# Kernel tuning notes

Measured on AMD Instinct MI355X. Metric: run time of the kernel, lower is better.

The kernel has to match this reference:

```python
import jax, jax.numpy as jnp
import numpy as np

N, M, D = 4096, 8192, 512

def setup_inputs() -> dict:
    key = jax.random.key(0)
    k1, k2, k3, k4 = jax.random.split(key, 4)
    X = jax.random.normal(k1, (N, D), dtype=jnp.float32)
    SV = jax.random.normal(k2, (M, D), dtype=jnp.float32)
    DC = jax.random.normal(k3, (1, M), dtype=jnp.float32)
    IC = jax.random.normal(k4, (1,), dtype=jnp.float32)
    gamma = jnp.float32(1.0 / D)
    return {"X": X, "SV": SV, "DC": DC, "IC": IC, "gamma": gamma}

def reference(X, SV, DC, IC, gamma):
    # Squared pairwise L2 distances via GEMM expansion (same math as
    # ||SV - x||^2 without materializing the [N, M, D] broadcast tensor):
    # d2[n, m] = ||x_n||^2 + ||sv_m||^2 - 2 * x_n . sv_m
    x2 = jnp.sum(X * X, axis=1)          # [N]
    sv2 = jnp.sum(SV * SV, axis=1)       # [M]
    cross = jnp.einsum("nd,md->nm", X, SV)  # [N, M]
    d2 = jnp.maximum(x2[:, None] + sv2[None, :] - 2.0 * cross, 0.0)
    k = jnp.exp(-gamma * d2)             # RBF kernel values [N, M]
    # Weighted reduction over support vectors + intercept -> decision values [N]
    return jnp.sum(k * DC, axis=1) + IC
```

## Files before the change

kernel.cpp:

```cpp
#include <hip/hip_runtime.h>
#include <stdint.h>

#define NN 4096
#define MM 8192
#define DD 512
#define KT 8

typedef __bf16 bf16x8 __attribute__((ext_vector_type(8)));
typedef __bf16 bf16x4 __attribute__((ext_vector_type(4)));
typedef float f32x4 __attribute__((ext_vector_type(4)));
typedef float f32x16 __attribute__((ext_vector_type(16)));

__device__ __forceinline__ void load_lds16(const void* g, void* l) {
  __builtin_amdgcn_global_load_lds(
      (const __attribute__((address_space(1))) unsigned int*)g,
      (__attribute__((address_space(3))) unsigned int*)l, 16, 0, 0);
}

__global__ __launch_bounds__(256) void convert_norm_kernel(
    const float* __restrict__ X, const float* __restrict__ SV,
    __bf16* __restrict__ Xb, __bf16* __restrict__ SVb,
    float* __restrict__ x2, float* __restrict__ sv2,
    float* __restrict__ out, const float* __restrict__ IC) {
  int wid = blockIdx.x * 4 + (threadIdx.x >> 6);
  int lane = threadIdx.x & 63;
  const float* src;
  __bf16* dst;
  float* nrm;
  if (wid < NN) {
    src = X + (size_t)wid * DD;
    dst = Xb + (size_t)wid * DD;
    nrm = x2 + wid;
    if (lane == 0) out[wid] = IC[0];
  } else {
    int r = wid - NN;
    src = SV + (size_t)r * DD;
    dst = SVb + (size_t)r * DD;
    nrm = sv2 + r;
  }
  const f32x4* s = (const f32x4*)src;
  f32x4 a = s[lane];
  f32x4 b = s[lane + 64];
  float sum = a.x * a.x + a.y * a.y + a.z * a.z + a.w * a.w +
              b.x * b.x + b.y * b.y + b.z * b.z + b.w * b.w;
  bf16x4 ca = {(__bf16)a.x, (__bf16)a.y, (__bf16)a.z, (__bf16)a.w};
  bf16x4 cb = {(__bf16)b.x, (__bf16)b.y, (__bf16)b.z, (__bf16)b.w};
  *(bf16x4*)(dst + 4 * lane) = ca;
  *(bf16x4*)(dst + 256 + 4 * lane) = cb;
#pragma unroll
  for (int m = 32; m >= 1; m >>= 1) sum += __shfl_xor(sum, m, 64);
  if (lane == 0) *nrm = sum;
}

__global__ __launch_bounds__(256, 4) void rbf_gemm_kernel(
    const bf16x8* __restrict__ Xb, const bf16x8* __restrict__ SVb,
    const float* __restrict__ x2, const float* __restrict__ sv2,
    const float* __restrict__ DC, const float* __restrict__ gamma_p,
    float* __restrict__ out) {
  __shared__ bf16x8 As[1024];
  __shared__ bf16x8 Bs[1024];

  const int t = threadIdx.x;
  const int lane = t & 63;
  const int wave = t >> 6;
  const int n0 = blockIdx.x * 128;
  const int m0 = blockIdx.y * 128;

  const int wave_m = wave & 1;
  const int wave_n = wave >> 1;
  const int l31 = lane & 31;
  const int lhi = lane >> 5;

  const int srow = t >> 3;
  const int sslot = t & 7;

  f32x16 acc[2][2];
#pragma unroll
  for (int i = 0; i < 2; ++i)
#pragma unroll
    for (int j = 0; j < 2; ++j)
#pragma unroll
      for (int r = 0; r < 16; ++r) acc[i][j][r] = 0.0f;

  for (int kt = 0; kt < KT; ++kt) {
#pragma unroll
    for (int it = 0; it < 4; ++it) {
      const int c = it * 256 + t;
      const int row = it * 32 + srow;
      const int kg = sslot ^ (row & 7);
      load_lds16(Xb + (size_t)(n0 + row) * 64 + kt * 8 + kg, &As[c]);
      load_lds16(SVb + (size_t)(m0 + row) * 64 + kt * 8 + kg, &Bs[c]);
    }
    __syncthreads();
#pragma unroll
    for (int ks = 0; ks < 4; ++ks) {
      const int kc = ks * 2 + lhi;
      const int sw = kc ^ (l31 & 7);
      const int ra = (wave_n * 64 + l31) * 8;
      const int rb = (wave_m * 64 + l31) * 8;
      bf16x8 af0 = As[ra + sw];
      bf16x8 af1 = As[ra + 256 + sw];
      bf16x8 bf0 = Bs[rb + sw];
      bf16x8 bf1 = Bs[rb + 256 + sw];
      acc[0][0] = __builtin_amdgcn_mfma_f32_32x32x16_bf16(af0, bf0, acc[0][0], 0, 0, 0);
      acc[0][1] = __builtin_amdgcn_mfma_f32_32x32x16_bf16(af0, bf1, acc[0][1], 0, 0, 0);
      acc[1][0] = __builtin_amdgcn_mfma_f32_32x32x16_bf16(af1, bf0, acc[1][0], 0, 0, 0);
      acc[1][1] = __builtin_amdgcn_mfma_f32_32x32x16_bf16(af1, bf1, acc[1][1], 0, 0, 0);
    }
    __syncthreads();
  }

  const float g = gamma_p[0];
  const float c2 = g * 1.4426950408889634f;

  float sv2v[2], dcv[2];
  const int colb = m0 + wave_m * 64 + l31;
  sv2v[0] = sv2[colb];
  dcv[0] = DC[colb];
  sv2v[1] = sv2[colb + 32];
  dcv[1] = DC[colb + 32];

#pragma unroll
  for (int i = 0; i < 2; ++i) {
    const int rowb = n0 + wave_n * 64 + i * 32 + 4 * lhi;
    float val[16];
#pragma unroll
    for (int g4 = 0; g4 < 4; ++g4) {
      f32x4 xv = *(const f32x4*)(x2 + rowb + 8 * g4);
#pragma unroll
      for (int r2 = 0; r2 < 4; ++r2) {
        const int reg = g4 * 4 + r2;
        float v = 0.0f;
#pragma unroll
        for (int j = 0; j < 2; ++j) {
          float d2 = xv[r2] + sv2v[j] - 2.0f * acc[i][j][reg];
          d2 = fmaxf(d2, 0.0f);
          v += exp2f(-c2 * d2) * dcv[j];
        }
        val[reg] = v;
      }
    }
#pragma unroll
    for (int m = 1; m < 32; m <<= 1)
#pragma unroll
      for (int reg = 0; reg < 16; ++reg)
        val[reg] += __shfl_xor(val[reg], m, 64);
    if (l31 == 0) {
#pragma unroll
      for (int g4 = 0; g4 < 4; ++g4)
#pragma unroll
        for (int r2 = 0; r2 < 4; ++r2)
          atomicAdd(&out[rowb + 8 * g4 + r2], val[g4 * 4 + r2]);
    }
  }
}

extern "C" void kernel_launch(void* const* d_in, const int* in_sizes, int n_in,
                              void* d_out, int out_size, void* d_ws, size_t ws_size,
                              hipStream_t stream) {
  const float* X = (const float*)d_in[0];
  const float* SV = (const float*)d_in[1];
  const float* DC = (const float*)d_in[2];
  const float* IC = (const float*)d_in[3];
  const float* gamma = (const float*)d_in[4];
  float* out = (float*)d_out;

  char* ws = (char*)d_ws;
  __bf16* Xb = (__bf16*)ws;
  __bf16* SVb = (__bf16*)(ws + (size_t)NN * DD * 2);
  float* x2 = (float*)(ws + (size_t)(NN + MM) * DD * 2);
  float* sv2 = x2 + NN;

  convert_norm_kernel<<<(NN + MM) / 4, 256, 0, stream>>>(X, SV, Xb, SVb, x2, sv2, out, IC);
  dim3 grid(NN / 128, MM / 128);
  rbf_gemm_kernel<<<grid, 256, 0, stream>>>((const bf16x8*)Xb, (const bf16x8*)SVb,
                                            x2, sv2, DC, gamma, out);
}
```

Baseline: 136.7 us.

## Double-buffer LDS tiles with half-depth K steps to overlap loads and MFMA

```diff
diff --git a/kernel.cpp b/kernel.cpp
--- a/kernel.cpp
+++ b/kernel.cpp
@@ -4,7 +4,7 @@
 #define NN 4096
 #define MM 8192
 #define DD 512
-#define KT 8
+#define KT2 16
 
 typedef __bf16 bf16x8 __attribute__((ext_vector_type(8)));
 typedef __bf16 bf16x4 __attribute__((ext_vector_type(4)));
@@ -57,8 +57,8 @@
     const float* __restrict__ x2, const float* __restrict__ sv2,
     const float* __restrict__ DC, const float* __restrict__ gamma_p,
     float* __restrict__ out) {
-  __shared__ bf16x8 As[1024];
-  __shared__ bf16x8 Bs[1024];
+  __shared__ bf16x8 As[2][512];
+  __shared__ bf16x8 Bs[2][512];
 
   const int t = threadIdx.x;
   const int lane = t & 63;
@@ -71,8 +71,17 @@
   const int l31 = lane & 31;
   const int lhi = lane >> 5;
 
-  const int srow = t >> 3;
-  const int sslot = t & 7;
+  const int c0 = t;
+  const int c1 = t + 256;
+  const int r0 = c0 >> 2, k0 = (c0 & 3) ^ (r0 & 3);
+  const int r1 = c1 >> 2, k1 = (c1 & 3) ^ (r1 & 3);
+  const size_t gA0 = (size_t)(n0 + r0) * 64 + k0;
+  const size_t gA1 = (size_t)(n0 + r1) * 64 + k1;
+  const size_t gB0 = (size_t)(m0 + r0) * 64 + k0;
+  const size_t gB1 = (size_t)(m0 + r1) * 64 + k1;
+
+  const int ra4 = (wave_n * 64 + l31) * 4;
+  const int rb4 = (wave_m * 64 + l31) * 4;
 
   f32x16 acc[2][2];
 #pragma unroll
@@ -82,26 +91,31 @@
 #pragma unroll
       for (int r = 0; r < 16; ++r) acc[i][j][r] = 0.0f;
 
-  for (int kt = 0; kt < KT; ++kt) {
+  load_lds16(Xb + gA0, &As[0][c0]);
+  load_lds16(Xb + gA1, &As[0][c1]);
+  load_lds16(SVb + gB0, &Bs[0][c0]);
+  load_lds16(SVb + gB1, &Bs[0][c1]);
+  __syncthreads();
+
 #pragma unroll
-    for (int it = 0; it < 4; ++it) {
-      const int c = it * 256 + t;
-      const int row = it * 32 + srow;
-      const int kg = sslot ^ (row & 7);
-      load_lds16(Xb + (size_t)(n0 + row) * 64 + kt * 8 + kg, &As[c]);
-      load_lds16(SVb + (size_t)(m0 + row) * 64 + kt * 8 + kg, &Bs[c]);
+  for (int kt = 0; kt < KT2; ++kt) {
+    const int cur = kt & 1;
+    const int nxt = cur ^ 1;
+    if (kt + 1 < KT2) {
+      const int ko = (kt + 1) * 4;
+      load_lds16(Xb + gA0 + ko, &As[nxt][c0]);
+      load_lds16(Xb + gA1 + ko, &As[nxt][c1]);
+      load_lds16(SVb + gB0 + ko, &Bs[nxt][c0]);
+      load_lds16(SVb + gB1 + ko, &Bs[nxt][c1]);
     }
-    __syncthreads();
 #pragma unroll
-    for (int ks = 0; ks < 4; ++ks) {
+    for (int ks = 0; ks < 2; ++ks) {
       const int kc = ks * 2 + lhi;
-      const int sw = kc ^ (l31 & 7);
-      const int ra = (wave_n * 64 + l31) * 8;
-      const int rb = (wave_m * 64 + l31) * 8;
-      bf16x8 af0 = As[ra + sw];
-      bf16x8 af1 = As[ra + 256 + sw];
-      bf16x8 bf0 = Bs[rb + sw];
-      bf16x8 bf1 = Bs[rb + 256 + sw];
+      const int sw = kc ^ (l31 & 3);
+      bf16x8 af0 = As[cur][ra4 + sw];
+      bf16x8 af1 = As[cur][ra4 + 128 + sw];
+      bf16x8 bf0 = Bs[cur][rb4 + sw];
+      bf16x8 bf1 = Bs[cur][rb4 + 128 + sw];
       acc[0][0] = __builtin_amdgcn_mfma_f32_32x32x16_bf16(af0, bf0, acc[0][0], 0, 0, 0);
       acc[0][1] = __builtin_amdgcn_mfma_f32_32x32x16_bf16(af0, bf1, acc[0][1], 0, 0, 0);
       acc[1][0] = __builtin_amdgcn_mfma_f32_32x32x16_bf16(af1, bf0, acc[1][0], 0, 0, 0);
```

Result: slower. 144.5 us (+5.7%).
